# Performance work log

Hardware: AMD Instinct MI355X
Metric: run time of the kernel (lower is better)

The kernel has to match this reference:

```python
import jax, jax.numpy as jnp
import numpy as np

N = 100000   # nodes
E = 1600000  # edges
IN = 128
HID = 128    # 2 * out_channels
OUT = 64


def setup_inputs() -> dict:
    key = jax.random.key(0)
    ks = jax.random.split(key, 8)
    x = jax.random.normal(ks[0], (N, IN), dtype=jnp.float32)
    edge_index = jax.random.randint(ks[1], (2, E), 0, N, dtype=jnp.int32)
    s = 1.0 / np.sqrt(IN)
    W1 = jax.random.normal(ks[2], (IN, HID), dtype=jnp.float32) * s
    Wm1 = jax.random.normal(ks[3], (HID, HID), dtype=jnp.float32) * s
    Wm2 = jax.random.normal(ks[4], (HID, HID), dtype=jnp.float32) * s
    W2 = jax.random.normal(ks[5], (HID, OUT), dtype=jnp.float32) * s
    b1 = jnp.zeros((HID,), jnp.float32)
    bm1 = jnp.zeros((HID,), jnp.float32)
    bm2 = jnp.zeros((HID,), jnp.float32)
    b2 = jnp.zeros((OUT,), jnp.float32)
    return {"x": x, "edge_index": edge_index, "W1": W1, "b1": b1,
            "Wm1": Wm1, "bm1": bm1, "Wm2": Wm2, "bm2": bm2,
            "W2": W2, "b2": b2}


def _gcn_norm(edge_index, num_nodes):
    # PyG GCNConv: add self-loops (weight 1), symmetric normalization.
    loop = jnp.arange(num_nodes, dtype=edge_index.dtype)
    src = jnp.concatenate([edge_index[0], loop])
    dst = jnp.concatenate([edge_index[1], loop])
    deg = jax.ops.segment_sum(jnp.ones_like(src, jnp.float32), dst,
                              num_segments=num_nodes)
    dinv = jnp.where(deg > 0, jax.lax.rsqrt(deg), 0.0)
    norm = dinv[src] * dinv[dst]  # [E + N]
    return src, dst, norm


def _gcn_conv(h, W, b, src, dst, norm, num_nodes):
    h = h @ W                                # dense transform [N, F_out]
    msg = h[src] * norm[:, None]             # gather + scale   [E+N, F_out]
    out = jax.ops.segment_sum(msg, dst, num_segments=num_nodes)  # scatter-add
    return out + b


def reference(x, edge_index, W1, b1, Wm1, bm1, Wm2, bm2, W2, b2):
    num_nodes = x.shape[0]
    src, dst, norm = _gcn_norm(edge_index, num_nodes)
    h = jax.nn.relu(_gcn_conv(x, W1, b1, src, dst, norm, num_nodes))
    h = jax.nn.relu(_gcn_conv(h, Wm1, bm1, src, dst, norm, num_nodes))
    h = jax.nn.relu(_gcn_conv(h, Wm2, bm2, src, dst, norm, num_nodes))
    return _gcn_conv(h, W2, b2, src, dst, norm, num_nodes)  # [N, OUT]
```

## Files before the change

kernel.cpp:

```cpp
#include <hip/hip_runtime.h>
#include <hip/hip_bf16.h>
#include <hip/hip_fp16.h>


#define NNODES 100000
#define NEDGES 1600000
#define NBUCK 782

typedef __attribute__((ext_vector_type(8))) _Float16 f16x8;
typedef __attribute__((ext_vector_type(4))) float f32x4;


__device__ inline float2 h2f2(unsigned int u) {
    __half2 h = *reinterpret_cast<__half2*>(&u);
    return __half22float2(h);
}
__device__ inline unsigned int f22h2(float a, float b) {
    __half2 h = __floats2half2_rn(a, b);
    return *reinterpret_cast<unsigned int*>(&h);
}

__device__ inline void split_h(float x, __half& h, __half& l) {
    h = __float2half(x);
    l = __float2half(x - __half2float(h));
}


__global__ void zero_ints(int* p, int n) {
    int i = blockIdx.x * blockDim.x + threadIdx.x;
    if (i < n) p[i] = 0;
}

__global__ __launch_bounds__(256) void hist_pass(const int* __restrict__ dst,
                                                 int* __restrict__ cnt, int e) {
    __shared__ int h[NBUCK];
    int tid = threadIdx.x;
    for (int i = tid; i < NBUCK; i += 256) h[i] = 0;
    __syncthreads();
    int base_e = blockIdx.x * 4096;
#pragma unroll
    for (int j = 0; j < 16; j++) {
        int i = base_e + j * 256 + tid;
        if (i < e) atomicAdd(&h[dst[i] >> 7], 1);
    }
    __syncthreads();
    for (int b = tid; b < NBUCK; b += 256)
        if (h[b]) atomicAdd(&cnt[b], h[b]);
}

__device__ inline void wfrag_one(const float* W, unsigned short* hi, unsigned short* lo,
                                 int e, int NT, int Ncols) {
    int j = e & 7;
    int l = (e >> 3) & 63;
    int t = (e >> 9) % NT;
    int c = e / (512 * NT);
    int k = c * 32 + (l >> 4) * 8 + j;
    int n = t * 16 + (l & 15);
    float x = W[k * Ncols + n];
    __half h, lw; split_h(x, h, lw);
    hi[e] = *(unsigned short*)&h;
    lo[e] = *(unsigned short*)&lw;
}

__global__ __launch_bounds__(256) void aux_kernel(
        const float* W1, unsigned short* hi1, unsigned short* lo1,
        const float* Wm1, unsigned short* him1, unsigned short* lom1,
        const float* Wm2, unsigned short* him2, unsigned short* lom2,
        const float* W2, unsigned short* hi2, unsigned short* lo2,
        const int* __restrict__ cnt, int* __restrict__ base, int e) {
    int blk = blockIdx.x;
    int tid = threadIdx.x;
    if (blk < 64)        { wfrag_one(W1,  hi1,  lo1,  blk * 256 + tid,         8, 128); return; }
    if (blk < 128)       { wfrag_one(Wm1, him1, lom1, (blk - 64) * 256 + tid,  8, 128); return; }
    if (blk < 192)       { wfrag_one(Wm2, him2, lom2, (blk - 128) * 256 + tid, 8, 128); return; }
    if (blk < 224)       { wfrag_one(W2,  hi2,  lo2,  (blk - 192) * 256 + tid, 4, 64);  return; }
    __shared__ int sd[256];
    int t = tid;
    int v[4]; int s = 0;
#pragma unroll
    for (int j = 0; j < 4; j++) {
        int i = t * 4 + j;
        v[j] = (i < NBUCK) ? cnt[i] : 0;
        s += v[j];
    }
    sd[t] = s; __syncthreads();
    for (int off = 1; off < 256; off <<= 1) {
        int x = (t >= off) ? sd[t - off] : 0;
        __syncthreads();
        sd[t] += x;
        __syncthreads();
    }
    int run = sd[t] - s;
#pragma unroll
    for (int j = 0; j < 4; j++) {
        int i = t * 4 + j;
        if (i < NBUCK) base[i] = run;
        run += v[j];
    }
    if (t == 0) base[NBUCK] = e;
}

__global__ void copy_fill(const int* __restrict__ base, int* __restrict__ fill) {
    int i = blockIdx.x * blockDim.x + threadIdx.x;
    if (i < NBUCK) fill[i] = base[i];
}

__global__ __launch_bounds__(256) void scatter_pass(const int* __restrict__ src,
                                                    const int* __restrict__ dst,
                                                    int* __restrict__ fill,
                                                    unsigned int* __restrict__ epart, int e) {
    __shared__ int h[NBUCK];
    int tid = threadIdx.x;
    for (int i = tid; i < NBUCK; i += 256) h[i] = 0;
    __syncthreads();
    int base_e = blockIdx.x * 4096;
#pragma unroll
    for (int j = 0; j < 16; j++) {
        int i = base_e + j * 256 + tid;
        if (i < e) atomicAdd(&h[dst[i] >> 7], 1);
    }
    __syncthreads();
    for (int b = tid; b < NBUCK; b += 256)
        if (h[b]) h[b] = atomicAdd(&fill[b], h[b]);
    __syncthreads();
#pragma unroll
    for (int j = 0; j < 16; j++) {
        int i = base_e + j * 256 + tid;
        if (i < e) {
            int d = dst[i];
            int bk = d >> 7;
            int pos = atomicAdd(&h[bk], 1);
            epart[pos] = ((unsigned int)src[i] << 7) | (unsigned int)(d & 127);
        }
    }
}

__global__ __launch_bounds__(256) void build_csr(const unsigned int* __restrict__ epart,
                                                 const int* __restrict__ base,
                                                 int* __restrict__ row_ptr,
                                                 int* __restrict__ col,
                                                 float* __restrict__ dinv,
                                                 int n, int e_total) {
    __shared__ int deg[128], degl[128], off[128], fil[256];
    int b = blockIdx.x, tid = threadIdx.x;
    int node0 = b << 7;
    int nn = n - node0; if (nn > 128) nn = 128;
    int e0 = base[b], e1 = base[b + 1];
    int cnt = e1 - e0;
    const int HALF = NNODES / 2;

    if (tid < 128) { deg[tid] = 0; degl[tid] = 0; }
    __syncthreads();
    for (int i = tid; i < cnt; i += 256) {
        unsigned int u = epart[e0 + i];
        int ld = (int)(u & 127);
        atomicAdd(&deg[ld], 1);
        if ((int)(u >> 7) < HALF) atomicAdd(&degl[ld], 1);
    }
    __syncthreads();
    if (tid < 128) off[tid] = deg[tid];
    __syncthreads();
    for (int o = 1; o < 128; o <<= 1) {
        int x = (tid < 128 && tid >= o) ? off[tid - o] : 0;
        __syncthreads();
        if (tid < 128) off[tid] += x;
        __syncthreads();
    }
    if (tid < 128) {
        int row_start = e0 + off[tid] - deg[tid];
        fil[tid] = row_start;
        fil[128 + tid] = row_start + degl[tid];
        if (tid < nn) {
            row_ptr[node0 + tid] = row_start;
            dinv[node0 + tid] = rsqrtf((float)(deg[tid] + 1));
        }
    }
    if (b == 0 && tid == 0) row_ptr[n] = e_total;
    __syncthreads();
    for (int i = tid; i < cnt; i += 256) {
        unsigned int u = epart[e0 + i];
        int ld = (int)(u & 127);
        int srcv = (int)(u >> 7);
        int pos = atomicAdd(&fil[(srcv < HALF ? 0 : 128) + ld], 1);
        col[pos] = srcv;
    }
}


__global__ __launch_bounds__(256) void gemm_l1(const float* __restrict__ A,
                                               const unsigned short* __restrict__ gwhi,
                                               const unsigned short* __restrict__ gwlo,
                                               const float* __restrict__ dinv,
                                               __half* __restrict__ T, int nrows) {
    constexpr int NT = 8, BN = 128;
    constexpr int WFRAG = 4 * NT * 64 * 8;
    __shared__ __align__(16) unsigned short s_hi[WFRAG];
    __shared__ __align__(16) unsigned short s_lo[WFRAG];
    int tid = threadIdx.x;
    for (int i = tid; i < WFRAG / 8; i += 256) {
        ((uint4*)s_hi)[i] = ((const uint4*)gwhi)[i];
        ((uint4*)s_lo)[i] = ((const uint4*)gwlo)[i];
    }
    __syncthreads();

    int wave = tid >> 6, lane = tid & 63;
    int m = lane & 15, q = lane >> 4;
    long row0 = ((long)blockIdx.x * 4 + wave) * 32;
    if (row0 >= nrows) return;
    long rowa = row0 + m;
    bool hasb = (row0 + 16) < nrows;
    long rowb = hasb ? (row0 + 16 + m) : rowa;

    f32x4 acc[2][NT];
#pragma unroll
    for (int s = 0; s < 2; s++)
#pragma unroll
        for (int t = 0; t < NT; t++)
#pragma unroll
            for (int r = 0; r < 4; r++) acc[s][t][r] = 0.f;

#pragma unroll
    for (int c = 0; c < 4; c++) {
        f16x8 ah[2], al[2];
        const float* pa = A + rowa * 128 + c * 32 + q * 8;
        const float* pb = A + rowb * 128 + c * 32 + q * 8;
        float fa[8], fb[8];
        *(float4*)&fa[0] = *(const float4*)pa;
        *(float4*)&fa[4] = *(const float4*)(pa + 4);
        *(float4*)&fb[0] = *(const float4*)pb;
        *(float4*)&fb[4] = *(const float4*)(pb + 4);
#pragma unroll
        for (int i = 0; i < 8; i++) {
            __half h, l;
            split_h(fa[i], h, l); ah[0][i] = *(_Float16*)&h; al[0][i] = *(_Float16*)&l;
            split_h(fb[i], h, l); ah[1][i] = *(_Float16*)&h; al[1][i] = *(_Float16*)&l;
        }
#pragma unroll
        for (int t = 0; t < NT; t++) {
            f16x8 bhi = *(const f16x8*)(s_hi + ((c * NT + t) * 64 + lane) * 8);
            f16x8 blo = *(const f16x8*)(s_lo + ((c * NT + t) * 64 + lane) * 8);
#pragma unroll
            for (int s = 0; s < 2; s++) {
                acc[s][t] = __builtin_amdgcn_mfma_f32_16x16x32_f16(al[s], bhi, acc[s][t], 0, 0, 0);
                acc[s][t] = __builtin_amdgcn_mfma_f32_16x16x32_f16(ah[s], blo, acc[s][t], 0, 0, 0);
                acc[s][t] = __builtin_amdgcn_mfma_f32_16x16x32_f16(ah[s], bhi, acc[s][t], 0, 0, 0);
            }
        }
    }

#pragma unroll
    for (int s = 0; s < 2; s++) {
        if (s == 1 && !hasb) break;
#pragma unroll
        for (int r = 0; r < 4; r++) {
            long row = row0 + s * 16 + q * 4 + r;
            if (row < nrows) {
                float di = dinv[row];
#pragma unroll
                for (int t = 0; t < NT; t++)
                    T[row * BN + t * 16 + m] = __float2half(acc[s][t][r] * di);
            }
        }
    }
}


template <int BN>
__global__ __launch_bounds__(256) void gemm_f16(const __half* __restrict__ A,
                                                const unsigned short* __restrict__ gwhi,
                                                const unsigned short* __restrict__ gwlo,
                                                const float* __restrict__ dinv,
                                                __half* __restrict__ T, int nrows) {
    constexpr int NT = BN / 16;
    constexpr int WFRAG = 4 * NT * 64 * 8;
    __shared__ __align__(16) unsigned short s_hi[WFRAG];
    __shared__ __align__(16) unsigned short s_lo[WFRAG];
    int tid = threadIdx.x;
    for (int i = tid; i < WFRAG / 8; i += 256) {
        ((uint4*)s_hi)[i] = ((const uint4*)gwhi)[i];
        ((uint4*)s_lo)[i] = ((const uint4*)gwlo)[i];
    }
    __syncthreads();

    int wave = tid >> 6, lane = tid & 63;
    int m = lane & 15, q = lane >> 4;
    long row0 = ((long)blockIdx.x * 4 + wave) * 32;
    if (row0 >= nrows) return;
    long rowa = row0 + m;
    bool hasb = (row0 + 16) < nrows;
    long rowb = hasb ? (row0 + 16 + m) : rowa;

    f32x4 acc[2][NT];
#pragma unroll
    for (int s = 0; s < 2; s++)
#pragma unroll
        for (int t = 0; t < NT; t++)
#pragma unroll
            for (int r = 0; r < 4; r++) acc[s][t][r] = 0.f;

#pragma unroll
    for (int c = 0; c < 4; c++) {
        f16x8 a[2];
        uint4 ra = *(const uint4*)(A + rowa * 128 + c * 32 + q * 8);
        uint4 rb = *(const uint4*)(A + rowb * 128 + c * 32 + q * 8);
        *(uint4*)&a[0] = ra;
        *(uint4*)&a[1] = rb;
#pragma unroll
        for (int t = 0; t < NT; t++) {
            f16x8 bhi = *(const f16x8*)(s_hi + ((c * NT + t) * 64 + lane) * 8);
            f16x8 blo = *(const f16x8*)(s_lo + ((c * NT + t) * 64 + lane) * 8);
#pragma unroll
            for (int s = 0; s < 2; s++) {
                acc[s][t] = __builtin_amdgcn_mfma_f32_16x16x32_f16(a[s], blo, acc[s][t], 0, 0, 0);
                acc[s][t] = __builtin_amdgcn_mfma_f32_16x16x32_f16(a[s], bhi, acc[s][t], 0, 0, 0);
            }
        }
    }

#pragma unroll
    for (int s = 0; s < 2; s++) {
        if (s == 1 && !hasb) break;
#pragma unroll
        for (int r = 0; r < 4; r++) {
            long row = row0 + s * 16 + q * 4 + r;
            if (row < nrows) {
                float di = dinv[row];
#pragma unroll
                for (int t = 0; t < NT; t++)
                    T[row * BN + t * 16 + m] = __float2half(acc[s][t][r] * di);
            }
        }
    }
}


__device__ inline void acc8(float* a, uint4 v) {
    float2 f0 = h2f2(v.x), f1 = h2f2(v.y), f2 = h2f2(v.z), f3 = h2f2(v.w);
    a[0] += f0.x; a[1] += f0.y; a[2] += f1.x; a[3] += f1.y;
    a[4] += f2.x; a[5] += f2.y; a[6] += f3.x; a[7] += f3.y;
}
__device__ inline void acc4(float* a, uint2 v) {
    float2 f0 = h2f2(v.x), f1 = h2f2(v.y);
    a[0] += f0.x; a[1] += f0.y; a[2] += f1.x; a[3] += f1.y;
}

__global__ __launch_bounds__(1024) void agg128h(const __half* __restrict__ t,
                                                const int* __restrict__ row_ptr,
                                                const int* __restrict__ col,
                                                const float* __restrict__ dinv,
                                                const float* __restrict__ bias,
                                                __half* __restrict__ out, int n) {
    int wave = threadIdx.x >> 6, lane = threadIdx.x & 63;
    int node = blockIdx.x * 16 + wave;
    if (node >= n) return;
    int q = lane >> 4, i = lane & 15;
    int r0 = row_ptr[node], r1 = row_ptr[node + 1];
    const uint4* t4 = (const uint4*)t;

    float a0[8], a1[8], a2[8], a3[8];
#pragma unroll
    for (int k = 0; k < 8; k++) { a0[k] = 0.f; a1[k] = 0.f; a2[k] = 0.f; a3[k] = 0.f; }

    int p = r0;
    for (; p + 16 <= r1; p += 16) {
        int c0 = col[p + q];
        int c1 = col[p + 4 + q];
        int c2 = col[p + 8 + q];
        int c3 = col[p + 12 + q];
        uint4 v0 = t4[(size_t)c0 * 16 + i];
        uint4 v1 = t4[(size_t)c1 * 16 + i];
        uint4 v2 = t4[(size_t)c2 * 16 + i];
        uint4 v3 = t4[(size_t)c3 * 16 + i];
        acc8(a0, v0); acc8(a1, v1); acc8(a2, v2); acc8(a3, v3);
    }
    for (; p + 8 <= r1; p += 8) {
        int c0 = col[p + q];
        int c1 = col[p + 4 + q];
        uint4 v0 = t4[(size_t)c0 * 16 + i];
        uint4 v1 = t4[(size_t)c1 * 16 + i];
        acc8(a0, v0); acc8(a1, v1);
    }
    for (; p < r1; p += 4) {
        int idx = p + q;
        if (idx < r1) {
            int c = col[idx];
            acc8(a0, t4[(size_t)c * 16 + i]);
        }
    }

    float s[8];
#pragma unroll
    for (int k = 0; k < 8; k++) s[k] = (a0[k] + a1[k]) + (a2[k] + a3[k]);
#pragma unroll
    for (int k = 0; k < 8; k++) s[k] += __shfl_xor(s[k], 16);
#pragma unroll
    for (int k = 0; k < 8; k++) s[k] += __shfl_xor(s[k], 32);

    if (q == 0) {
        uint4 ownv = t4[(size_t)node * 16 + i];
        float own[8];
        float2 f0 = h2f2(ownv.x), f1 = h2f2(ownv.y), f2 = h2f2(ownv.z), f3 = h2f2(ownv.w);
        own[0] = f0.x; own[1] = f0.y; own[2] = f1.x; own[3] = f1.y;
        own[4] = f2.x; own[5] = f2.y; own[6] = f3.x; own[7] = f3.y;
        float di = dinv[node];
        float4 bA = ((const float4*)bias)[i * 2];
        float4 bB = ((const float4*)bias)[i * 2 + 1];
        float o[8];
        o[0] = di * (s[0] + own[0]) + bA.x;
        o[1] = di * (s[1] + own[1]) + bA.y;
        o[2] = di * (s[2] + own[2]) + bA.z;
        o[3] = di * (s[3] + own[3]) + bA.w;
        o[4] = di * (s[4] + own[4]) + bB.x;
        o[5] = di * (s[5] + own[5]) + bB.y;
        o[6] = di * (s[6] + own[6]) + bB.z;
        o[7] = di * (s[7] + own[7]) + bB.w;
#pragma unroll
        for (int k = 0; k < 8; k++) o[k] = fmaxf(o[k], 0.f);
        uint4 ov;
        ov.x = f22h2(o[0], o[1]); ov.y = f22h2(o[2], o[3]);
        ov.z = f22h2(o[4], o[5]); ov.w = f22h2(o[6], o[7]);
        ((uint4*)out)[(size_t)node * 16 + i] = ov;
    }
}

__global__ __launch_bounds__(1024) void agg64h(const __half* __restrict__ t,
                                               const int* __restrict__ row_ptr,
                                               const int* __restrict__ col,
                                               const float* __restrict__ dinv,
                                               const float* __restrict__ bias,
                                               float* __restrict__ out, int n) {
    int wave = threadIdx.x >> 6, lane = threadIdx.x & 63;
    int node = blockIdx.x * 16 + wave;
    if (node >= n) return;
    int q = lane >> 4, i = lane & 15;
    int r0 = row_ptr[node], r1 = row_ptr[node + 1];
    const uint2* t2 = (const uint2*)t;

    float a0[4], a1[4], a2[4], a3[4];
#pragma unroll
    for (int k = 0; k < 4; k++) { a0[k] = 0.f; a1[k] = 0.f; a2[k] = 0.f; a3[k] = 0.f; }

    int p = r0;
    for (; p + 16 <= r1; p += 16) {
        int c0 = col[p + q];
        int c1 = col[p + 4 + q];
        int c2 = col[p + 8 + q];
        int c3 = col[p + 12 + q];
        uint2 v0 = t2[(size_t)c0 * 16 + i];
        uint2 v1 = t2[(size_t)c1 * 16 + i];
        uint2 v2 = t2[(size_t)c2 * 16 + i];
        uint2 v3 = t2[(size_t)c3 * 16 + i];
        acc4(a0, v0); acc4(a1, v1); acc4(a2, v2); acc4(a3, v3);
    }
    for (; p + 8 <= r1; p += 8) {
        int c0 = col[p + q];
        int c1 = col[p + 4 + q];
        uint2 v0 = t2[(size_t)c0 * 16 + i];
        uint2 v1 = t2[(size_t)c1 * 16 + i];
        acc4(a0, v0); acc4(a1, v1);
    }
    for (; p < r1; p += 4) {
        int idx = p + q;
        if (idx < r1) {
            int c = col[idx];
            acc4(a0, t2[(size_t)c * 16 + i]);
        }
    }

    float s[4];
#pragma unroll
    for (int k = 0; k < 4; k++) s[k] = (a0[k] + a1[k]) + (a2[k] + a3[k]);
#pragma unroll
    for (int k = 0; k < 4; k++) s[k] += __shfl_xor(s[k], 16);
#pragma unroll
    for (int k = 0; k < 4; k++) s[k] += __shfl_xor(s[k], 32);

    if (q == 0) {
        uint2 ownv = t2[(size_t)node * 16 + i];
        float own[4];
        float2 f0 = h2f2(ownv.x), f1 = h2f2(ownv.y);
        own[0] = f0.x; own[1] = f0.y; own[2] = f1.x; own[3] = f1.y;
        float di = dinv[node];
        float4 b4 = ((const float4*)bias)[i];
        float4 o;
        o.x = di * (s[0] + own[0]) + b4.x;
        o.y = di * (s[1] + own[1]) + b4.y;
        o.z = di * (s[2] + own[2]) + b4.z;
        o.w = di * (s[3] + own[3]) + b4.w;
        ((float4*)out)[(size_t)node * 16 + i] = o;
    }
}


extern "C" void kernel_launch(void* const* d_in, const int* in_sizes, int n_in,
                              void* d_out, int out_size, void* d_ws, size_t ws_size,
                              hipStream_t stream) {
    const int N = NNODES, E = NEDGES;
    const float* x   = (const float*)d_in[0];
    const int*   ei  = (const int*)d_in[1];
    const int*   src = ei;
    const int*   dst = ei + E;
    const float* W1  = (const float*)d_in[2];
    const float* b1  = (const float*)d_in[3];
    const float* Wm1 = (const float*)d_in[4];
    const float* bm1 = (const float*)d_in[5];
    const float* Wm2 = (const float*)d_in[6];
    const float* bm2 = (const float*)d_in[7];
    const float* W2  = (const float*)d_in[8];
    const float* b2  = (const float*)d_in[9];
    float* out = (float*)d_out;

    int* bucket_cnt  = (int*)d_ws;
    int* bucket_base = bucket_cnt + 784;
    int* bucket_fill = bucket_base + 784;
    int* row_ptr     = bucket_fill + 784;
    int* col         = row_ptr + (N + 4);
    unsigned int* epart = (unsigned int*)(col + E);
    float* dinv  = (float*)(epart + E);
    __half* t16  = (__half*)(dinv + N);
    __half* bufA = t16 + (size_t)N * 128;
    unsigned short* whi1  = (unsigned short*)(bufA + (size_t)N * 128);
    unsigned short* wlo1  = whi1 + 16384;
    unsigned short* whiM1 = wlo1 + 16384;
    unsigned short* wloM1 = whiM1 + 16384;
    unsigned short* whiM2 = wloM1 + 16384;
    unsigned short* wloM2 = whiM2 + 16384;
    unsigned short* whi2  = wloM2 + 16384;
    unsigned short* wlo2  = whi2 + 8192;

    const int EB4 = (E + 4095) / 4096;

    zero_ints<<<4, 256, 0, stream>>>(bucket_cnt, NBUCK);
    hist_pass<<<EB4, 256, 0, stream>>>(dst, bucket_cnt, E);
    aux_kernel<<<225, 256, 0, stream>>>(W1, whi1, wlo1, Wm1, whiM1, wloM1,
                                        Wm2, whiM2, wloM2, W2, whi2, wlo2,
                                        bucket_cnt, bucket_base, E);
    copy_fill<<<4, 256, 0, stream>>>(bucket_base, bucket_fill);
    scatter_pass<<<EB4, 256, 0, stream>>>(src, dst, bucket_fill, epart, E);
    build_csr<<<NBUCK, 256, 0, stream>>>(epart, bucket_base, row_ptr, col, dinv, N, E);

    const int GB = (N + 127) / 128;
    const int AB = (N + 15) / 16;

    gemm_l1<<<GB, 256, 0, stream>>>(x, whi1, wlo1, dinv, t16, N);
    agg128h<<<AB, 1024, 0, stream>>>(t16, row_ptr, col, dinv, b1, bufA, N);

    gemm_f16<128><<<GB, 256, 0, stream>>>(bufA, whiM1, wloM1, dinv, t16, N);
    agg128h<<<AB, 1024, 0, stream>>>(t16, row_ptr, col, dinv, bm1, bufA, N);

    gemm_f16<128><<<GB, 256, 0, stream>>>(bufA, whiM2, wloM2, dinv, t16, N);
    agg128h<<<AB, 1024, 0, stream>>>(t16, row_ptr, col, dinv, bm2, bufA, N);

    gemm_f16<64><<<GB, 256, 0, stream>>>(bufA, whi2, wlo2, dinv, t16, N);
    agg64h<<<AB, 1024, 0, stream>>>(t16, row_ptr, col, dinv, b2, out, N);
}
```

Measured before the change: 620.4 us.

## Store features in column-sliced layout and aggregate per 16-column slice

Changes the intermediate fp16 feature matrices from row-major to a sliced layout of 16-column blocks ([slice][node][16]). The GEMMs now write this layout and read it back, and the aggregation kernels give each block one slice across four nodes. Each slice table is smaller, so the random gathers are meant to hit L2 more often. The build_csr half-split ordering of source columns is dropped, and col loads and stores become nontemporal. In exchange, each node's col list is read once per slice, and the gathers are narrower 4-byte loads.

```diff
diff --git a/kernel.cpp b/kernel.cpp
--- a/kernel.cpp
+++ b/kernel.cpp
@@ -141,22 +141,17 @@
                                                  int* __restrict__ col,
                                                  float* __restrict__ dinv,
                                                  int n, int e_total) {
-    __shared__ int deg[128], degl[128], off[128], fil[256];
+    __shared__ int deg[128], off[128], fil[128];
     int b = blockIdx.x, tid = threadIdx.x;
     int node0 = b << 7;
     int nn = n - node0; if (nn > 128) nn = 128;
     int e0 = base[b], e1 = base[b + 1];
     int cnt = e1 - e0;
-    const int HALF = NNODES / 2;
-
-    if (tid < 128) { deg[tid] = 0; degl[tid] = 0; }
-    __syncthreads();
-    for (int i = tid; i < cnt; i += 256) {
-        unsigned int u = epart[e0 + i];
-        int ld = (int)(u & 127);
-        atomicAdd(&deg[ld], 1);
-        if ((int)(u >> 7) < HALF) atomicAdd(&degl[ld], 1);
-    }
+
+    if (tid < 128) deg[tid] = 0;
+    __syncthreads();
+    for (int i = tid; i < cnt; i += 256)
+        atomicAdd(&deg[epart[e0 + i] & 127], 1);
     __syncthreads();
     if (tid < 128) off[tid] = deg[tid];
     __syncthreads();
@@ -167,11 +162,10 @@
         __syncthreads();
     }
     if (tid < 128) {
-        int row_start = e0 + off[tid] - deg[tid];
-        fil[tid] = row_start;
-        fil[128 + tid] = row_start + degl[tid];
+        int ex = e0 + off[tid] - deg[tid];
+        fil[tid] = ex;
         if (tid < nn) {
-            row_ptr[node0 + tid] = row_start;
+            row_ptr[node0 + tid] = ex;
             dinv[node0 + tid] = rsqrtf((float)(deg[tid] + 1));
         }
     }
@@ -180,9 +174,8 @@
     for (int i = tid; i < cnt; i += 256) {
         unsigned int u = epart[e0 + i];
         int ld = (int)(u & 127);
-        int srcv = (int)(u >> 7);
-        int pos = atomicAdd(&fil[(srcv < HALF ? 0 : 128) + ld], 1);
-        col[pos] = srcv;
+        int pos = atomicAdd(&fil[ld], 1);
+        col[pos] = (int)(u >> 7);
     }
 }
 
@@ -192,7 +185,7 @@
                                                const unsigned short* __restrict__ gwlo,
                                                const float* __restrict__ dinv,
                                                __half* __restrict__ T, int nrows) {
-    constexpr int NT = 8, BN = 128;
+    constexpr int NT = 8;
     constexpr int WFRAG = 4 * NT * 64 * 8;
     __shared__ __align__(16) unsigned short s_hi[WFRAG];
     __shared__ __align__(16) unsigned short s_lo[WFRAG];
@@ -258,7 +251,7 @@
                 float di = dinv[row];
 #pragma unroll
                 for (int t = 0; t < NT; t++)
-                    T[row * BN + t * 16 + m] = __float2half(acc[s][t][r] * di);
+                    T[((size_t)t * nrows + row) * 16 + m] = __float2half(acc[s][t][r] * di);
             }
         }
     }
@@ -300,11 +293,11 @@
 
 #pragma unroll
     for (int c = 0; c < 4; c++) {
+        int isl = 2 * c + (q >> 1);
+        int ioff = (q & 1) * 8;
         f16x8 a[2];
-        uint4 ra = *(const uint4*)(A + rowa * 128 + c * 32 + q * 8);
-        uint4 rb = *(const uint4*)(A + rowb * 128 + c * 32 + q * 8);
-        *(uint4*)&a[0] = ra;
-        *(uint4*)&a[1] = rb;
+        *(uint4*)&a[0] = *(const uint4*)(A + ((size_t)isl * nrows + rowa) * 16 + ioff);
+        *(uint4*)&a[1] = *(const uint4*)(A + ((size_t)isl * nrows + rowb) * 16 + ioff);
 #pragma unroll
         for (int t = 0; t < NT; t++) {
             f16x8 bhi = *(const f16x8*)(s_hi + ((c * NT + t) * 64 + lane) * 8);
@@ -327,167 +320,111 @@
                 float di = dinv[row];
 #pragma unroll
                 for (int t = 0; t < NT; t++)
-                    T[row * BN + t * 16 + m] = __float2half(acc[s][t][r] * di);
+                    T[((size_t)t * nrows + row) * 16 + m] = __float2half(acc[s][t][r] * di);
             }
         }
     }
 }
 
 
-__device__ inline void acc8(float* a, uint4 v) {
-    float2 f0 = h2f2(v.x), f1 = h2f2(v.y), f2 = h2f2(v.z), f3 = h2f2(v.w);
-    a[0] += f0.x; a[1] += f0.y; a[2] += f1.x; a[3] += f1.y;
-    a[4] += f2.x; a[5] += f2.y; a[6] += f3.x; a[7] += f3.y;
-}
-__device__ inline void acc4(float* a, uint2 v) {
-    float2 f0 = h2f2(v.x), f1 = h2f2(v.y);
-    a[0] += f0.x; a[1] += f0.y; a[2] += f1.x; a[3] += f1.y;
-}
-
-__global__ __launch_bounds__(1024) void agg128h(const __half* __restrict__ t,
-                                                const int* __restrict__ row_ptr,
-                                                const int* __restrict__ col,
-                                                const float* __restrict__ dinv,
-                                                const float* __restrict__ bias,
-                                                __half* __restrict__ out, int n) {
-    int wave = threadIdx.x >> 6, lane = threadIdx.x & 63;
-    int node = blockIdx.x * 16 + wave;
-    if (node >= n) return;
-    int q = lane >> 4, i = lane & 15;
-    int r0 = row_ptr[node], r1 = row_ptr[node + 1];
-    const uint4* t4 = (const uint4*)t;
-
-    float a0[8], a1[8], a2[8], a3[8];
-#pragma unroll
-    for (int k = 0; k < 8; k++) { a0[k] = 0.f; a1[k] = 0.f; a2[k] = 0.f; a3[k] = 0.f; }
-
-    int p = r0;
-    for (; p + 16 <= r1; p += 16) {
-        int c0 = col[p + q];
-        int c1 = col[p + 4 + q];
-        int c2 = col[p + 8 + q];
-        int c3 = col[p + 12 + q];
-        uint4 v0 = t4[(size_t)c0 * 16 + i];
-        uint4 v1 = t4[(size_t)c1 * 16 + i];
-        uint4 v2 = t4[(size_t)c2 * 16 + i];
-        uint4 v3 = t4[(size_t)c3 * 16 + i];
-        acc8(a0, v0); acc8(a1, v1); acc8(a2, v2); acc8(a3, v3);
-    }
-    for (; p + 8 <= r1; p += 8) {
-        int c0 = col[p + q];
-        int c1 = col[p + 4 + q];
-        uint4 v0 = t4[(size_t)c0 * 16 + i];
-        uint4 v1 = t4[(size_t)c1 * 16 + i];
-        acc8(a0, v0); acc8(a1, v1);
-    }
-    for (; p < r1; p += 4) {
-        int idx = p + q;
-        if (idx < r1) {
-            int c = col[idx];
-            acc8(a0, t4[(size_t)c * 16 + i]);
-        }
-    }
-
-    float s[8];
-#pragma unroll
-    for (int k = 0; k < 8; k++) s[k] = (a0[k] + a1[k]) + (a2[k] + a3[k]);
-#pragma unroll
-    for (int k = 0; k < 8; k++) s[k] += __shfl_xor(s[k], 16);
-#pragma unroll
-    for (int k = 0; k < 8; k++) s[k] += __shfl_xor(s[k], 32);
-
-    if (q == 0) {
-        uint4 ownv = t4[(size_t)node * 16 + i];
-        float own[8];
-        float2 f0 = h2f2(ownv.x), f1 = h2f2(ownv.y), f2 = h2f2(ownv.z), f3 = h2f2(ownv.w);
-        own[0] = f0.x; own[1] = f0.y; own[2] = f1.x; own[3] = f1.y;
-        own[4] = f2.x; own[5] = f2.y; own[6] = f3.x; own[7] = f3.y;
-        float di = dinv[node];
-        float4 bA = ((const float4*)bias)[i * 2];
-        float4 bB = ((const float4*)bias)[i * 2 + 1];
-        float o[8];
-        o[0] = di * (s[0] + own[0]) + bA.x;
-        o[1] = di * (s[1] + own[1]) + bA.y;
-        o[2] = di * (s[2] + own[2]) + bA.z;
-        o[3] = di * (s[3] + own[3]) + bA.w;
-        o[4] = di * (s[4] + own[4]) + bB.x;
-        o[5] = di * (s[5] + own[5]) + bB.y;
-        o[6] = di * (s[6] + own[6]) + bB.z;
-        o[7] = di * (s[7] + own[7]) + bB.w;
-#pragma unroll
-        for (int k = 0; k < 8; k++) o[k] = fmaxf(o[k], 0.f);
-        uint4 ov;
-        ov.x = f22h2(o[0], o[1]); ov.y = f22h2(o[2], o[3]);
-        ov.z = f22h2(o[4], o[5]); ov.w = f22h2(o[6], o[7]);
-        ((uint4*)out)[(size_t)node * 16 + i] = ov;
-    }
-}
-
-__global__ __launch_bounds__(1024) void agg64h(const __half* __restrict__ t,
+__global__ __launch_bounds__(256) void agg128s(const __half* __restrict__ t,
                                                const int* __restrict__ row_ptr,
                                                const int* __restrict__ col,
                                                const float* __restrict__ dinv,
                                                const float* __restrict__ bias,
-                                               float* __restrict__ out, int n) {
+                                               __half* __restrict__ out, int n) {
     int wave = threadIdx.x >> 6, lane = threadIdx.x & 63;
-    int node = blockIdx.x * 16 + wave;
+    int slice = blockIdx.x & 7;
+    int node = (blockIdx.x >> 3) * 4 + wave;
     if (node >= n) return;
-    int q = lane >> 4, i = lane & 15;
+    int q = lane >> 3, i = lane & 7;
     int r0 = row_ptr[node], r1 = row_ptr[node + 1];
-    const uint2* t2 = (const uint2*)t;
-
-    float a0[4], a1[4], a2[4], a3[4];
-#pragma unroll
-    for (int k = 0; k < 4; k++) { a0[k] = 0.f; a1[k] = 0.f; a2[k] = 0.f; a3[k] = 0.f; }
-
+    const unsigned int* tbl = (const unsigned int*)t + (size_t)slice * n * 8 + i;
+
+    float s0 = 0.f, s1 = 0.f, u0 = 0.f, u1 = 0.f;
     int p = r0;
     for (; p + 16 <= r1; p += 16) {
-        int c0 = col[p + q];
-        int c1 = col[p + 4 + q];
-        int c2 = col[p + 8 + q];
-        int c3 = col[p + 12 + q];
-        uint2 v0 = t2[(size_t)c0 * 16 + i];
-        uint2 v1 = t2[(size_t)c1 * 16 + i];
-        uint2 v2 = t2[(size_t)c2 * 16 + i];
-        uint2 v3 = t2[(size_t)c3 * 16 + i];
-        acc4(a0, v0); acc4(a1, v1); acc4(a2, v2); acc4(a3, v3);
+        int c0 = __builtin_nontemporal_load(col + p + q);
+        int c1 = __builtin_nontemporal_load(col + p + 8 + q);
+        unsigned int v0 = tbl[(size_t)c0 * 8];
+        unsigned int v1 = tbl[(size_t)c1 * 8];
+        float2 f0 = h2f2(v0), f1 = h2f2(v1);
+        s0 += f0.x; s1 += f0.y; u0 += f1.x; u1 += f1.y;
     }
     for (; p + 8 <= r1; p += 8) {
-        int c0 = col[p + q];
-        int c1 = col[p + 4 + q];
-        uint2 v0 = t2[(size_t)c0 * 16 + i];
-        uint2 v1 = t2[(size_t)c1 * 16 + i];
-        acc4(a0, v0); acc4(a1, v1);
-    }
-    for (; p < r1; p += 4) {
-        int idx = p + q;
-        if (idx < r1) {
-            int c = col[idx];
-            acc4(a0, t2[(size_t)c * 16 + i]);
-        }
-    }
-
-    float s[4];
-#pragma unroll
-    for (int k = 0; k < 4; k++) s[k] = (a0[k] + a1[k]) + (a2[k] + a3[k]);
-#pragma unroll
-    for (int k = 0; k < 4; k++) s[k] += __shfl_xor(s[k], 16);
-#pragma unroll
-    for (int k = 0; k < 4; k++) s[k] += __shfl_xor(s[k], 32);
+        int c0 = __builtin_nontemporal_load(col + p + q);
+        float2 f0 = h2f2(tbl[(size_t)c0 * 8]);
+        s0 += f0.x; s1 += f0.y;
+    }
+    if (p + q < r1) {
+        int c0 = __builtin_nontemporal_load(col + p + q);
+        float2 f0 = h2f2(tbl[(size_t)c0 * 8]);
+        s0 += f0.x; s1 += f0.y;
+    }
+    s0 += u0; s1 += u1;
+    s0 += __shfl_xor(s0, 8);  s1 += __shfl_xor(s1, 8);
+    s0 += __shfl_xor(s0, 16); s1 += __shfl_xor(s1, 16);
+    s0 += __shfl_xor(s0, 32); s1 += __shfl_xor(s1, 32);
 
     if (q == 0) {
-        uint2 ownv = t2[(size_t)node * 16 + i];
-        float own[4];
-        float2 f0 = h2f2(ownv.x), f1 = h2f2(ownv.y);
-        own[0] = f0.x; own[1] = f0.y; own[2] = f1.x; own[3] = f1.y;
+        float2 own = h2f2(tbl[(size_t)node * 8]);
         float di = dinv[node];
-        float4 b4 = ((const float4*)bias)[i];
-        float4 o;
-        o.x = di * (s[0] + own[0]) + b4.x;
-        o.y = di * (s[1] + own[1]) + b4.y;
-        o.z = di * (s[2] + own[2]) + b4.z;
-        o.w = di * (s[3] + own[3]) + b4.w;
-        ((float4*)out)[(size_t)node * 16 + i] = o;
+        float2 b = *(const float2*)(bias + slice * 16 + i * 2);
+        float o0 = di * (s0 + own.x) + b.x;
+        float o1 = di * (s1 + own.y) + b.y;
+        o0 = fmaxf(o0, 0.f); o1 = fmaxf(o1, 0.f);
+        __builtin_nontemporal_store(f22h2(o0, o1),
+            (unsigned int*)out + (size_t)slice * n * 8 + (size_t)node * 8 + i);
+    }
+}
+
+__global__ __launch_bounds__(256) void agg64s(const __half* __restrict__ t,
+                                              const int* __restrict__ row_ptr,
+                                              const int* __restrict__ col,
+                                              const float* __restrict__ dinv,
+                                              const float* __restrict__ bias,
+                                              float* __restrict__ out, int n) {
+    int wave = threadIdx.x >> 6, lane = threadIdx.x & 63;
+    int slice = blockIdx.x & 3;
+    int node = (blockIdx.x >> 2) * 4 + wave;
+    if (node >= n) return;
+    int q = lane >> 3, i = lane & 7;
+    int r0 = row_ptr[node], r1 = row_ptr[node + 1];
+    const unsigned int* tbl = (const unsigned int*)t + (size_t)slice * n * 8 + i;
+
+    float s0 = 0.f, s1 = 0.f, u0 = 0.f, u1 = 0.f;
+    int p = r0;
+    for (; p + 16 <= r1; p += 16) {
+        int c0 = __builtin_nontemporal_load(col + p + q);
+        int c1 = __builtin_nontemporal_load(col + p + 8 + q);
+        unsigned int v0 = tbl[(size_t)c0 * 8];
+        unsigned int v1 = tbl[(size_t)c1 * 8];
+        float2 f0 = h2f2(v0), f1 = h2f2(v1);
+        s0 += f0.x; s1 += f0.y; u0 += f1.x; u1 += f1.y;
+    }
+    for (; p + 8 <= r1; p += 8) {
+        int c0 = __builtin_nontemporal_load(col + p + q);
+        float2 f0 = h2f2(tbl[(size_t)c0 * 8]);
+        s0 += f0.x; s1 += f0.y;
+    }
+    if (p + q < r1) {
+        int c0 = __builtin_nontemporal_load(col + p + q);
+        float2 f0 = h2f2(tbl[(size_t)c0 * 8]);
+        s0 += f0.x; s1 += f0.y;
+    }
+    s0 += u0; s1 += u1;
+    s0 += __shfl_xor(s0, 8);  s1 += __shfl_xor(s1, 8);
+    s0 += __shfl_xor(s0, 16); s1 += __shfl_xor(s1, 16);
+    s0 += __shfl_xor(s0, 32); s1 += __shfl_xor(s1, 32);
+
+    if (q == 0) {
+        float2 own = h2f2(tbl[(size_t)node * 8]);
+        float di = dinv[node];
+        float2 b = *(const float2*)(bias + slice * 16 + i * 2);
+        float2 o;
+        o.x = di * (s0 + own.x) + b.x;
+        o.y = di * (s1 + own.y) + b.y;
+        *(float2*)(out + (size_t)node * 64 + slice * 16 + i * 2) = o;
     }
 }
 
@@ -539,18 +476,20 @@
     scatter_pass<<<EB4, 256, 0, stream>>>(src, dst, bucket_fill, epart, E);
     build_csr<<<NBUCK, 256, 0, stream>>>(epart, bucket_base, row_ptr, col, dinv, N, E);
 
-    const int GB = (N + 127) / 128;
-    const int AB = (N + 15) / 16;
+    const int GB  = (N + 127) / 128;
+    const int NC  = (N + 3) / 4;
+    const int AB8 = NC * 8;
+    const int AB4 = NC * 4;
 
     gemm_l1<<<GB, 256, 0, stream>>>(x, whi1, wlo1, dinv, t16, N);
-    agg128h<<<AB, 1024, 0, stream>>>(t16, row_ptr, col, dinv, b1, bufA, N);
+    agg128s<<<AB8, 256, 0, stream>>>(t16, row_ptr, col, dinv, b1, bufA, N);
 
     gemm_f16<128><<<GB, 256, 0, stream>>>(bufA, whiM1, wloM1, dinv, t16, N);
-    agg128h<<<AB, 1024, 0, stream>>>(t16, row_ptr, col, dinv, bm1, bufA, N);
+    agg128s<<<AB8, 256, 0, stream>>>(t16, row_ptr, col, dinv, bm1, bufA, N);
 
     gemm_f16<128><<<GB, 256, 0, stream>>>(bufA, whiM2, wloM2, dinv, t16, N);
-    agg128h<<<AB, 1024, 0, stream>>>(t16, row_ptr, col, dinv, bm2, bufA, N);
+    agg128s<<<AB8, 256, 0, stream>>>(t16, row_ptr, col, dinv, bm2, bufA, N);
 
     gemm_f16<64><<<GB, 256, 0, stream>>>(bufA, whi2, wlo2, dinv, t16, N);
-    agg64h<<<AB, 1024, 0, stream>>>(t16, row_ptr, col, dinv, b2, out, N);
-}
+    agg64s<<<AB4, 256, 0, stream>>>(t16, row_ptr, col, dinv, b2, out, N);
+}
```

After: 1.164 ms. +87.7%, slower.

## Unroll aggregation gathers to eight masked loads per iteration with smaller blocks

Applied to the files above, without the earlier changes.

The aggregation kernels replace the 16/8/4-edge tiered loops with a single loop that issues eight independent masked gathers per iteration, using clamped indices and a 0/1 multiplier so there are no tail branches. This raises memory-level parallelism per wave. Block size drops from 1024 to 256 threads (4 nodes per block), which may help scheduling and tail balance. build_csr also stops splitting each row by source half (which had ordered columns for locality) and drops the extra shared-memory counters; this simplifies CSR construction but may reduce cache locality in the gathers.

```diff
diff --git a/kernel.cpp b/kernel.cpp
--- a/kernel.cpp
+++ b/kernel.cpp
@@ -23,6 +23,19 @@
 __device__ inline void split_h(float x, __half& h, __half& l) {
     h = __float2half(x);
     l = __float2half(x - __half2float(h));
+}
+
+__device__ inline void accm8(float* a, uint4 v, float m) {
+    float2 f0 = h2f2(v.x), f1 = h2f2(v.y), f2 = h2f2(v.z), f3 = h2f2(v.w);
+    a[0] = fmaf(m, f0.x, a[0]); a[1] = fmaf(m, f0.y, a[1]);
+    a[2] = fmaf(m, f1.x, a[2]); a[3] = fmaf(m, f1.y, a[3]);
+    a[4] = fmaf(m, f2.x, a[4]); a[5] = fmaf(m, f2.y, a[5]);
+    a[6] = fmaf(m, f3.x, a[6]); a[7] = fmaf(m, f3.y, a[7]);
+}
+__device__ inline void accm4(float* a, uint2 v, float m) {
+    float2 f0 = h2f2(v.x), f1 = h2f2(v.y);
+    a[0] = fmaf(m, f0.x, a[0]); a[1] = fmaf(m, f0.y, a[1]);
+    a[2] = fmaf(m, f1.x, a[2]); a[3] = fmaf(m, f1.y, a[3]);
 }
 
 
@@ -141,22 +154,17 @@
                                                  int* __restrict__ col,
                                                  float* __restrict__ dinv,
                                                  int n, int e_total) {
-    __shared__ int deg[128], degl[128], off[128], fil[256];
+    __shared__ int deg[128], off[128], fil[128];
     int b = blockIdx.x, tid = threadIdx.x;
     int node0 = b << 7;
     int nn = n - node0; if (nn > 128) nn = 128;
     int e0 = base[b], e1 = base[b + 1];
     int cnt = e1 - e0;
-    const int HALF = NNODES / 2;
-
-    if (tid < 128) { deg[tid] = 0; degl[tid] = 0; }
-    __syncthreads();
-    for (int i = tid; i < cnt; i += 256) {
-        unsigned int u = epart[e0 + i];
-        int ld = (int)(u & 127);
-        atomicAdd(&deg[ld], 1);
-        if ((int)(u >> 7) < HALF) atomicAdd(&degl[ld], 1);
-    }
+
+    if (tid < 128) deg[tid] = 0;
+    __syncthreads();
+    for (int i = tid; i < cnt; i += 256)
+        atomicAdd(&deg[epart[e0 + i] & 127], 1);
     __syncthreads();
     if (tid < 128) off[tid] = deg[tid];
     __syncthreads();
@@ -167,11 +175,10 @@
         __syncthreads();
     }
     if (tid < 128) {
-        int row_start = e0 + off[tid] - deg[tid];
-        fil[tid] = row_start;
-        fil[128 + tid] = row_start + degl[tid];
+        int ex = e0 + off[tid] - deg[tid];
+        fil[tid] = ex;
         if (tid < nn) {
-            row_ptr[node0 + tid] = row_start;
+            row_ptr[node0 + tid] = ex;
             dinv[node0 + tid] = rsqrtf((float)(deg[tid] + 1));
         }
     }
@@ -180,9 +187,8 @@
     for (int i = tid; i < cnt; i += 256) {
         unsigned int u = epart[e0 + i];
         int ld = (int)(u & 127);
-        int srcv = (int)(u >> 7);
-        int pos = atomicAdd(&fil[(srcv < HALF ? 0 : 128) + ld], 1);
-        col[pos] = srcv;
+        int pos = atomicAdd(&fil[ld], 1);
+        col[pos] = (int)(u >> 7);
     }
 }
 
@@ -301,10 +307,8 @@
 #pragma unroll
     for (int c = 0; c < 4; c++) {
         f16x8 a[2];
-        uint4 ra = *(const uint4*)(A + rowa * 128 + c * 32 + q * 8);
-        uint4 rb = *(const uint4*)(A + rowb * 128 + c * 32 + q * 8);
-        *(uint4*)&a[0] = ra;
-        *(uint4*)&a[1] = rb;
+        *(uint4*)&a[0] = *(const uint4*)(A + rowa * 128 + c * 32 + q * 8);
+        *(uint4*)&a[1] = *(const uint4*)(A + rowb * 128 + c * 32 + q * 8);
 #pragma unroll
         for (int t = 0; t < NT; t++) {
             f16x8 bhi = *(const f16x8*)(s_hi + ((c * NT + t) * 64 + lane) * 8);
@@ -334,24 +338,14 @@
 }
 
 
-__device__ inline void acc8(float* a, uint4 v) {
-    float2 f0 = h2f2(v.x), f1 = h2f2(v.y), f2 = h2f2(v.z), f3 = h2f2(v.w);
-    a[0] += f0.x; a[1] += f0.y; a[2] += f1.x; a[3] += f1.y;
-    a[4] += f2.x; a[5] += f2.y; a[6] += f3.x; a[7] += f3.y;
-}
-__device__ inline void acc4(float* a, uint2 v) {
-    float2 f0 = h2f2(v.x), f1 = h2f2(v.y);
-    a[0] += f0.x; a[1] += f0.y; a[2] += f1.x; a[3] += f1.y;
-}
-
-__global__ __launch_bounds__(1024) void agg128h(const __half* __restrict__ t,
-                                                const int* __restrict__ row_ptr,
-                                                const int* __restrict__ col,
-                                                const float* __restrict__ dinv,
-                                                const float* __restrict__ bias,
-                                                __half* __restrict__ out, int n) {
+__global__ __launch_bounds__(256) void agg128h(const __half* __restrict__ t,
+                                               const int* __restrict__ row_ptr,
+                                               const int* __restrict__ col,
+                                               const float* __restrict__ dinv,
+                                               const float* __restrict__ bias,
+                                               __half* __restrict__ out, int n) {
     int wave = threadIdx.x >> 6, lane = threadIdx.x & 63;
-    int node = blockIdx.x * 16 + wave;
+    int node = blockIdx.x * 4 + wave;
     if (node >= n) return;
     int q = lane >> 4, i = lane & 15;
     int r0 = row_ptr[node], r1 = row_ptr[node + 1];
@@ -361,31 +355,28 @@
 #pragma unroll
     for (int k = 0; k < 8; k++) { a0[k] = 0.f; a1[k] = 0.f; a2[k] = 0.f; a3[k] = 0.f; }
 
-    int p = r0;
-    for (; p + 16 <= r1; p += 16) {
-        int c0 = col[p + q];
-        int c1 = col[p + 4 + q];
-        int c2 = col[p + 8 + q];
-        int c3 = col[p + 12 + q];
-        uint4 v0 = t4[(size_t)c0 * 16 + i];
-        uint4 v1 = t4[(size_t)c1 * 16 + i];
-        uint4 v2 = t4[(size_t)c2 * 16 + i];
-        uint4 v3 = t4[(size_t)c3 * 16 + i];
-        acc8(a0, v0); acc8(a1, v1); acc8(a2, v2); acc8(a3, v3);
-    }
-    for (; p + 8 <= r1; p += 8) {
-        int c0 = col[p + q];
-        int c1 = col[p + 4 + q];
-        uint4 v0 = t4[(size_t)c0 * 16 + i];
-        uint4 v1 = t4[(size_t)c1 * 16 + i];
-        acc8(a0, v0); acc8(a1, v1);
-    }
-    for (; p < r1; p += 4) {
-        int idx = p + q;
-        if (idx < r1) {
-            int c = col[idx];
-            acc8(a0, t4[(size_t)c * 16 + i]);
-        }
+    for (int p = r0; p < r1; p += 32) {
+        int idx[8]; int c[8]; float mk[8];
+#pragma unroll
+        for (int s = 0; s < 8; s++) {
+            idx[s] = p + s * 4 + q;
+            bool v = idx[s] < r1;
+            int safe = v ? idx[s] : r0;
+            c[s] = col[safe];
+            mk[s] = v ? 1.f : 0.f;
+        }
+        uint4 g0 = t4[(size_t)c[0] * 16 + i];
+        uint4 g1 = t4[(size_t)c[1] * 16 + i];
+        uint4 g2 = t4[(size_t)c[2] * 16 + i];
+        uint4 g3 = t4[(size_t)c[3] * 16 + i];
+        uint4 g4 = t4[(size_t)c[4] * 16 + i];
+        uint4 g5 = t4[(size_t)c[5] * 16 + i];
+        uint4 g6 = t4[(size_t)c[6] * 16 + i];
+        uint4 g7 = t4[(size_t)c[7] * 16 + i];
+        accm8(a0, g0, mk[0]); accm8(a1, g1, mk[1]);
+        accm8(a2, g2, mk[2]); accm8(a3, g3, mk[3]);
+        accm8(a0, g4, mk[4]); accm8(a1, g5, mk[5]);
+        accm8(a2, g6, mk[6]); accm8(a3, g7, mk[7]);
     }
 
     float s[8];
@@ -406,14 +397,14 @@
         float4 bA = ((const float4*)bias)[i * 2];
         float4 bB = ((const float4*)bias)[i * 2 + 1];
         float o[8];
-        o[0] = di * (s[0] + own[0]) + bA.x;
-        o[1] = di * (s[1] + own[1]) + bA.y;
-        o[2] = di * (s[2] + own[2]) + bA.z;
-        o[3] = di * (s[3] + own[3]) + bA.w;
-        o[4] = di * (s[4] + own[4]) + bB.x;
-        o[5] = di * (s[5] + own[5]) + bB.y;
-        o[6] = di * (s[6] + own[6]) + bB.z;
-        o[7] = di * (s[7] + own[7]) + bB.w;
+        o[0] = fmaf(di, s[0] + own[0], bA.x);
+        o[1] = fmaf(di, s[1] + own[1], bA.y);
+        o[2] = fmaf(di, s[2] + own[2], bA.z);
+        o[3] = fmaf(di, s[3] + own[3], bA.w);
+        o[4] = fmaf(di, s[4] + own[4], bB.x);
+        o[5] = fmaf(di, s[5] + own[5], bB.y);
+        o[6] = fmaf(di, s[6] + own[6], bB.z);
+        o[7] = fmaf(di, s[7] + own[7], bB.w);
 #pragma unroll
         for (int k = 0; k < 8; k++) o[k] = fmaxf(o[k], 0.f);
         uint4 ov;
@@ -423,14 +414,14 @@
     }
 }
 
-__global__ __launch_bounds__(1024) void agg64h(const __half* __restrict__ t,
-                                               const int* __restrict__ row_ptr,
-                                               const int* __restrict__ col,
-                                               const float* __restrict__ dinv,
-                                               const float* __restrict__ bias,
-                                               float* __restrict__ out, int n) {
+__global__ __launch_bounds__(256) void agg64h(const __half* __restrict__ t,
+                                              const int* __restrict__ row_ptr,
+                                              const int* __restrict__ col,
+                                              const float* __restrict__ dinv,
+                                              const float* __restrict__ bias,
+                                              float* __restrict__ out, int n) {
     int wave = threadIdx.x >> 6, lane = threadIdx.x & 63;
-    int node = blockIdx.x * 16 + wave;
+    int node = blockIdx.x * 4 + wave;
     if (node >= n) return;
     int q = lane >> 4, i = lane & 15;
     int r0 = row_ptr[node], r1 = row_ptr[node + 1];
@@ -440,31 +431,28 @@
 #pragma unroll
     for (int k = 0; k < 4; k++) { a0[k] = 0.f; a1[k] = 0.f; a2[k] = 0.f; a3[k] = 0.f; }
 
-    int p = r0;
-    for (; p + 16 <= r1; p += 16) {
-        int c0 = col[p + q];
-        int c1 = col[p + 4 + q];
-        int c2 = col[p + 8 + q];
-        int c3 = col[p + 12 + q];
-        uint2 v0 = t2[(size_t)c0 * 16 + i];
-        uint2 v1 = t2[(size_t)c1 * 16 + i];
-        uint2 v2 = t2[(size_t)c2 * 16 + i];
-        uint2 v3 = t2[(size_t)c3 * 16 + i];
-        acc4(a0, v0); acc4(a1, v1); acc4(a2, v2); acc4(a3, v3);
-    }
-    for (; p + 8 <= r1; p += 8) {
-        int c0 = col[p + q];
-        int c1 = col[p + 4 + q];
-        uint2 v0 = t2[(size_t)c0 * 16 + i];
-        uint2 v1 = t2[(size_t)c1 * 16 + i];
-        acc4(a0, v0); acc4(a1, v1);
-    }
-    for (; p < r1; p += 4) {
-        int idx = p + q;
-        if (idx < r1) {
-            int c = col[idx];
-            acc4(a0, t2[(size_t)c * 16 + i]);
-        }
+    for (int p = r0; p < r1; p += 32) {
+        int idx[8]; int c[8]; float mk[8];
+#pragma unroll
+        for (int s = 0; s < 8; s++) {
+            idx[s] = p + s * 4 + q;
+            bool v = idx[s] < r1;
+            int safe = v ? idx[s] : r0;
+            c[s] = col[safe];
+            mk[s] = v ? 1.f : 0.f;
+        }
+        uint2 g0 = t2[(size_t)c[0] * 16 + i];
+        uint2 g1 = t2[(size_t)c[1] * 16 + i];
+        uint2 g2 = t2[(size_t)c[2] * 16 + i];
+        uint2 g3 = t2[(size_t)c[3] * 16 + i];
+        uint2 g4 = t2[(size_t)c[4] * 16 + i];
+        uint2 g5 = t2[(size_t)c[5] * 16 + i];
+        uint2 g6 = t2[(size_t)c[6] * 16 + i];
+        uint2 g7 = t2[(size_t)c[7] * 16 + i];
+        accm4(a0, g0, mk[0]); accm4(a1, g1, mk[1]);
+        accm4(a2, g2, mk[2]); accm4(a3, g3, mk[3]);
+        accm4(a0, g4, mk[4]); accm4(a1, g5, mk[5]);
+        accm4(a2, g6, mk[6]); accm4(a3, g7, mk[7]);
     }
 
     float s[4];
@@ -483,11 +471,11 @@
         float di = dinv[node];
         float4 b4 = ((const float4*)bias)[i];
         float4 o;
-        o.x = di * (s[0] + own[0]) + b4.x;
-        o.y = di * (s[1] + own[1]) + b4.y;
-        o.z = di * (s[2] + own[2]) + b4.z;
-        o.w = di * (s[3] + own[3]) + b4.w;
-        ((float4*)out)[(size_t)node * 16 + i] = o;
+        o.x = fmaf(di, s[0] + own[0], b4.x);
+        o.y = fmaf(di, s[1] + own[1], b4.y);
+        o.z = fmaf(di, s[2] + own[2], b4.z);
+        o.w = fmaf(di, s[3] + own[3], b4.w);
+        *(float4*)(out + (size_t)node * 64 + i * 4) = o;
     }
 }
 
@@ -540,17 +528,17 @@
     build_csr<<<NBUCK, 256, 0, stream>>>(epart, bucket_base, row_ptr, col, dinv, N, E);
 
     const int GB = (N + 127) / 128;
-    const int AB = (N + 15) / 16;
+    const int AB = (N + 3) / 4;
 
     gemm_l1<<<GB, 256, 0, stream>>>(x, whi1, wlo1, dinv, t16, N);
-    agg128h<<<AB, 1024, 0, stream>>>(t16, row_ptr, col, dinv, b1, bufA, N);
+    agg128h<<<AB, 256, 0, stream>>>(t16, row_ptr, col, dinv, b1, bufA, N);
 
     gemm_f16<128><<<GB, 256, 0, stream>>>(bufA, whiM1, wloM1, dinv, t16, N);
-    agg128h<<<AB, 1024, 0, stream>>>(t16, row_ptr, col, dinv, bm1, bufA, N);
+    agg128h<<<AB, 256, 0, stream>>>(t16, row_ptr, col, dinv, bm1, bufA, N);
 
     gemm_f16<128><<<GB, 256, 0, stream>>>(bufA, whiM2, wloM2, dinv, t16, N);
-    agg128h<<<AB, 1024, 0, stream>>>(t16, row_ptr, col, dinv, bm2, bufA, N);
+    agg128h<<<AB, 256, 0, stream>>>(t16, row_ptr, col, dinv, bm2, bufA, N);
 
     gemm_f16<64><<<GB, 256, 0, stream>>>(bufA, whi2, wlo2, dinv, t16, N);
-    agg64h<<<AB, 1024, 0, stream>>>(t16, row_ptr, col, dinv, b2, out, N);
-}
+    agg64h<<<AB, 256, 0, stream>>>(t16, row_ptr, col, dinv, b2, out, N);
+}
```

Result: faster. 540.6 us (-12.9%).
